# Kernel optimization log

Measured on AMD Instinct MI355X. Metric: run time of the kernel, lower is better.

The kernel has to match this reference:

```python
import jax, jax.numpy as jnp
import numpy as np
from jax import lax

SEQ_LEN = 256
INPUT_DIM = 1
HIDDEN = 1024
NUM_CLASSES = 10
BATCH = 512


def _kaiming_uniform(key, shape):
    # torch kaiming_uniform_ default: bound = sqrt(6 / fan_in), fan_in = shape[1]
    fan_in = shape[1]
    bound = float(np.sqrt(6.0 / fan_in))
    return jax.random.uniform(key, shape, jnp.float32, -bound, bound)


def setup_inputs() -> dict:
    key = jax.random.key(0)
    ks = jax.random.split(key, 16)
    inp = {"x": jax.random.normal(ks[0], (BATCH, SEQ_LEN), jnp.float32)}
    names_shapes = [
        ("Wgx", (HIDDEN, INPUT_DIM)), ("Wgh", (HIDDEN, HIDDEN)), ("bg", (HIDDEN, 1)),
        ("Wix", (HIDDEN, INPUT_DIM)), ("Wih", (HIDDEN, HIDDEN)), ("bi", (HIDDEN, 1)),
        ("Wfx", (HIDDEN, INPUT_DIM)), ("Wfh", (HIDDEN, HIDDEN)), ("bf", (HIDDEN, 1)),
        ("Wox", (HIDDEN, INPUT_DIM)), ("Woh", (HIDDEN, HIDDEN)), ("bo", (HIDDEN, 1)),
        ("Wph", (NUM_CLASSES, HIDDEN)), ("bp", (NUM_CLASSES, 1)),
    ]
    for k, (name, shape) in zip(ks[1:], names_shapes):
        inp[name] = _kaiming_uniform(k, shape)
    return inp


def reference(x, Wgx, Wgh, bg, Wix, Wih, bi, Wfx, Wfh, bf, Wox, Woh, bo, Wph, bp):
    B = x.shape[0]
    H = Wgh.shape[0]
    h0 = jnp.zeros((H, B), x.dtype)
    c0 = jnp.zeros((H, B), x.dtype)
    xs = x.T  # [S, B]; each step xt is [B] (input_dim == 1)

    def step(carry, xt):
        ht, ct = carry
        xt = xt[None, :]  # [1, B]
        g = jnp.tanh(Wgx @ xt + Wgh @ ht + bg)
        i = jax.nn.sigmoid(Wix @ xt + Wih @ ht + bi)
        f = jax.nn.sigmoid(Wfx @ xt + Wfh @ ht + bf)
        o = jax.nn.sigmoid(Wox @ xt + Woh @ ht + bo)
        ct = g * i + ct * f
        ht = jnp.tanh(ct) * o
        return (ht, ct), None

    (ht, ct), _ = lax.scan(step, (h0, c0), xs)
    pt = Wph @ ht + bp  # [num_classes, B], only last step's pt is returned
    return pt.T  # [B, num_classes]
```

## Files before the change

kernel.cpp:

```cpp
#include <hip/hip_runtime.h>


#define HID  1024
#define SEQL 256

typedef __bf16 bf16x8 __attribute__((ext_vector_type(8)));
typedef float  f32x16 __attribute__((ext_vector_type(16)));
typedef unsigned u32x4 __attribute__((ext_vector_type(4)));

#define AS1 __attribute__((address_space(1)))
#define AS3 __attribute__((address_space(3)))

__device__ __forceinline__ float fast_sigmoid(float v) {
    float e = __expf(-v);
    return 1.0f / (1.0f + e);
}
__device__ __forceinline__ float fast_tanh(float v) {
    float e = __expf(2.0f * v);
    return 1.0f - 2.0f / (e + 1.0f);
}
__device__ __forceinline__ unsigned pk2bf(float a, float b) {
    unsigned short ua = __builtin_bit_cast(unsigned short, (__bf16)a);
    unsigned short ub = __builtin_bit_cast(unsigned short, (__bf16)b);
    return (unsigned)ua | ((unsigned)ub << 16);
}
__device__ __forceinline__ float bfhi(unsigned u) { return __builtin_bit_cast(float, u & 0xFFFF0000u); }
__device__ __forceinline__ float bflo(unsigned u) { return __builtin_bit_cast(float, u << 16); }

__device__ __forceinline__ u32x4 load16_sc1(const void* p) {
    u32x4 r;
    asm volatile("global_load_dwordx4 %0, %1, off sc1\n\t"
                 "s_waitcnt vmcnt(0)"
                 : "=v"(r) : "v"(p) : "memory");
    return r;
}

__global__ __launch_bounds__(256) void lstm_init(unsigned short* htA, unsigned* flags, float* out) {
    int idx = blockIdx.x * 256 + threadIdx.x;
    uint4 z; z.x = 0; z.y = 0; z.z = 0; z.w = 0;
    ((uint4*)htA)[idx] = z;
    if (idx < 512) flags[idx] = 0;
    if (idx < 5120) out[idx] = 0.05f;
}

__global__ __attribute__((amdgpu_flat_work_group_size(256, 256), amdgpu_waves_per_eu(1, 1)))
void lstm_main(
    const float* __restrict__ x,
    const float* __restrict__ Wgx, const float* __restrict__ Wgh, const float* __restrict__ bg,
    const float* __restrict__ Wix, const float* __restrict__ Wih, const float* __restrict__ bi,
    const float* __restrict__ Wfx, const float* __restrict__ Wfh, const float* __restrict__ bf_,
    const float* __restrict__ Wox, const float* __restrict__ Woh, const float* __restrict__ bo,
    const float* __restrict__ Wph, const float* __restrict__ bp,
    float* __restrict__ out,
    unsigned short* __restrict__ htA, unsigned short* __restrict__ htB,
    unsigned* __restrict__ flags)
{
    extern __shared__ uint4 ldsB[];

    const int tid = threadIdx.x;
    const int w   = tid >> 6;
    const int l   = tid & 63;
    const int l31 = l & 31;
    const int h5  = l >> 5;
    const int gid = blockIdx.x;
    const int c   = gid & 7;
    const int r   = gid >> 3;

    const int gate = l31 >> 3;
    const int hrow = (r << 5) + (w << 3) + (l & 7);
    const float* Wsel = (gate == 0) ? Wgh : (gate == 1) ? Wih : (gate == 2) ? Wfh : Woh;
    const float* wrow = Wsel + hrow * HID + (h5 << 3);
    bf16x8 A[64];
#pragma unroll
    for (int kk = 0; kk < 64; ++kk) {
        const float4* p = (const float4*)(wrow + kk * 16);
        float4 u0 = p[0], u1 = p[1];
        bf16x8 a;
        a[0] = (__bf16)u0.x; a[1] = (__bf16)u0.y; a[2] = (__bf16)u0.z; a[3] = (__bf16)u0.w;
        a[4] = (__bf16)u1.x; a[5] = (__bf16)u1.y; a[6] = (__bf16)u1.z; a[7] = (__bf16)u1.w;
        A[kk] = a;
        __builtin_amdgcn_sched_barrier(0);
    }

    float wx16[16], bs16[16];
    {
        const float* WxA[4] = {Wgx, Wix, Wfx, Wox};
        const float* bA[4]  = {bg, bi, bf_, bo};
#pragma unroll
        for (int j = 0; j < 16; ++j) {
            int g = j >> 2;
            int h = (r << 5) + (w << 3) + (j & 3) + (h5 << 2);
            wx16[j] = WxA[g][h];
            bs16[j] = bA[g][h];
        }
    }

    float ct[8];
#pragma unroll
    for (int i = 0; i < 8; ++i) ct[i] = 0.f;

    const unsigned short* htR = htA;
    unsigned short*       htW = htB;
    unsigned* gflags = flags + (c << 6);
    const float* xrow0 = x + (unsigned)((c << 6) + l31) * SEQL;
    const float* xrow1 = x + (unsigned)((c << 6) + 32 + l31) * SEQL;

    float xv0 = xrow0[0], xv1 = xrow1[0];

    for (int t = 0; t < SEQL; ++t) {
        const unsigned short* gR = htR + (c << 16);

#pragma unroll
        for (int ch = 0; ch < 4; ++ch) {
#pragma unroll
            for (int j = 0; j < 8; ++j) {
                int q = (w << 3) + j;
                const void* g = (const void*)(gR + ch * 16384 + q * 512 + (l << 3));
                __builtin_amdgcn_global_load_lds((const AS1 void*)g,
                    (AS3 void*)&ldsB[(ch * 32 + q) * 64], 16, 0, 0x10 );
            }
        }
        __builtin_amdgcn_sched_barrier(0);
        int tn = (t + 1 < SEQL) ? t + 1 : t;
        float nx0 = xrow0[tn], nx1 = xrow1[tn];
        __builtin_amdgcn_sched_barrier(0);

        f32x16 acc0, acc1;
#pragma unroll
        for (int j = 0; j < 16; ++j) {
            acc0[j] = fmaf(wx16[j], xv0, bs16[j]);
            acc1[j] = fmaf(wx16[j], xv1, bs16[j]);
        }

#pragma unroll
        for (int ch = 0; ch < 4; ++ch) {
            if      (ch == 0) asm volatile("s_waitcnt vmcnt(24)" ::: "memory");
            else if (ch == 1) asm volatile("s_waitcnt vmcnt(16)" ::: "memory");
            else if (ch == 2) asm volatile("s_waitcnt vmcnt(8)"  ::: "memory");
            else              asm volatile("s_waitcnt vmcnt(2)"  ::: "memory");
            __builtin_amdgcn_s_barrier();
            asm volatile("" ::: "memory");
#pragma unroll
            for (int kk = 0; kk < 16; ++kk) {
                bf16x8 b0 = __builtin_bit_cast(bf16x8, ldsB[(ch * 32 + kk * 2 + 0) * 64 + l]);
                bf16x8 b1 = __builtin_bit_cast(bf16x8, ldsB[(ch * 32 + kk * 2 + 1) * 64 + l]);
                acc0 = __builtin_amdgcn_mfma_f32_32x32x16_bf16(A[ch * 16 + kk], b0, acc0, 0, 0, 0);
                acc1 = __builtin_amdgcn_mfma_f32_32x32x16_bf16(A[ch * 16 + kk], b1, acc1, 0, 0, 0);
            }
        }

        float htv[8];
#pragma unroll
        for (int nt = 0; nt < 2; ++nt) {
            f32x16 ac = nt ? acc1 : acc0;
#pragma unroll
            for (int d = 0; d < 4; ++d) {
                float g  = fast_tanh(ac[d]);
                float ii = fast_sigmoid(ac[4 + d]);
                float ff = fast_sigmoid(ac[8 + d]);
                float oo = fast_sigmoid(ac[12 + d]);
                float cc = fmaf(ct[nt * 4 + d], ff, g * ii);
                ct[nt * 4 + d] = cc;
                htv[nt * 4 + d] = fast_tanh(cc) * oo;
            }
        }

        {
            unsigned short* gW = htW + (c << 16);
            int kkw  = (r << 1) + (w >> 1);
            int slot = ((w & 1) << 5) + l31;
#pragma unroll
            for (int nt = 0; nt < 2; ++nt) {
                unsigned lo = pk2bf(htv[nt * 4 + 0], htv[nt * 4 + 1]);
                unsigned hi = pk2bf(htv[nt * 4 + 2], htv[nt * 4 + 3]);
                unsigned long long v = (unsigned long long)lo | ((unsigned long long)hi << 32);
                unsigned long long* dst =
                    (unsigned long long*)(gW + (((kkw * 2 + nt) * 64 + slot) * 8 + (h5 << 2)));
                __hip_atomic_store(dst, v, __ATOMIC_RELAXED, __HIP_MEMORY_SCOPE_AGENT);
            }
        }

        asm volatile("s_waitcnt vmcnt(0)" ::: "memory");
        __syncthreads();
        unsigned target = (unsigned)(t + 1);
        if (tid == 0)
            __hip_atomic_store(&gflags[r], target, __ATOMIC_RELAXED, __HIP_MEMORY_SCOPE_AGENT);
        if (w == 0) {
            const unsigned* fp = gflags + l31;
            while (true) {
                unsigned v = __hip_atomic_load(fp, __ATOMIC_RELAXED, __HIP_MEMORY_SCOPE_AGENT);
                if (__ballot(v >= target) == ~0ull) break;
                __builtin_amdgcn_s_sleep(1);
            }
        }
        __syncthreads();

        xv0 = nx0; xv1 = nx1;
        const unsigned short* tmp = htR; htR = htW; htW = (unsigned short*)tmp;
    }

    {
        const unsigned short* hfin = htR + (c << 16);
        for (int p = w; p < 20; p += 4) {
            int bloc = (r << 1) + (p / 10);
            int bb   = (c << 6) + bloc;
            int cls  = p % 10;
            const unsigned short* base = hfin + l * 1024 + ((bloc >> 5) & 1) * 512
                                              + (bloc & 31) * 8;
            u32x4 u0 = load16_sc1(base);
            u32x4 u1 = load16_sc1(base + 256);
            const float* wp = Wph + (unsigned)cls * HID + (unsigned)l * 16;
            float s = 0.f;
#pragma unroll
            for (int e = 0; e < 4; ++e) {
                s = fmaf(wp[2 * e],         bflo(u0[e]), s);
                s = fmaf(wp[2 * e + 1],     bfhi(u0[e]), s);
                s = fmaf(wp[8 + 2 * e],     bflo(u1[e]), s);
                s = fmaf(wp[8 + 2 * e + 1], bfhi(u1[e]), s);
            }
#pragma unroll
            for (int off = 32; off > 0; off >>= 1) s += __shfl_xor(s, off, 64);
            if (l == 0) out[bb * 10 + cls] = s + bp[cls];
        }
    }
}

extern "C" void kernel_launch(void* const* d_in, const int* in_sizes, int n_in,
                              void* d_out, int out_size, void* d_ws, size_t ws_size,
                              hipStream_t stream) {
    const float* x   = (const float*)d_in[0];
    const float* Wgx = (const float*)d_in[1];
    const float* Wgh = (const float*)d_in[2];
    const float* bg  = (const float*)d_in[3];
    const float* Wix = (const float*)d_in[4];
    const float* Wih = (const float*)d_in[5];
    const float* bi  = (const float*)d_in[6];
    const float* Wfx = (const float*)d_in[7];
    const float* Wfh = (const float*)d_in[8];
    const float* bf_ = (const float*)d_in[9];
    const float* Wox = (const float*)d_in[10];
    const float* Woh = (const float*)d_in[11];
    const float* bo  = (const float*)d_in[12];
    const float* Wph = (const float*)d_in[13];
    const float* bp  = (const float*)d_in[14];
    float* out = (float*)d_out;

    char* ws = (char*)d_ws;
    unsigned short* htA = (unsigned short*)ws;
    unsigned short* htB = (unsigned short*)(ws + (1 << 20));
    unsigned*     flags = (unsigned*)(ws + (2 << 20));

    lstm_init<<<dim3(256), dim3(256), 0, stream>>>(htA, flags, out);

    static int lds_set = 0;
    if (!lds_set) {
        hipFuncSetAttribute((const void*)lstm_main,
                            hipFuncAttributeMaxDynamicSharedMemorySize, 131072);
        lds_set = 1;
    }
    lstm_main<<<dim3(256), dim3(256), 131072, stream>>>(
        x, Wgx, Wgh, bg, Wix, Wih, bi, Wfx, Wfh, bf_,
        Wox, Woh, bo, Wph, bp, out, htA, htB, flags);
}
```

Before: 2.142 ms.

## Replace per-step block barriers with per-wave flags polled by every wave

The cross-workgroup handshake changes from one flag per workgroup, polled by wave 0 between two __syncthreads, to one flag per wave. Each wave polls all flags of its batch column with 64-bit loads at the start of the next step, and a final poll is added before the projection. Both __syncthreads per timestep are removed, and the hidden-state and flag stores become atomic exchanges. The aim is to cut intra-block barrier and serial-polling latency on the recurrent critical path, at the cost of more polling traffic and finer ordering that LDS and buffer reuse now depend on.

```diff
diff --git a/kernel.cpp b/kernel.cpp
--- a/kernel.cpp
+++ b/kernel.cpp
@@ -39,7 +39,7 @@
     int idx = blockIdx.x * 256 + threadIdx.x;
     uint4 z; z.x = 0; z.y = 0; z.z = 0; z.w = 0;
     ((uint4*)htA)[idx] = z;
-    if (idx < 512) flags[idx] = 0;
+    if (idx < 1024) flags[idx] = 0;
     if (idx < 5120) out[idx] = 0.05f;
 }
 
@@ -101,13 +101,26 @@
 
     const unsigned short* htR = htA;
     unsigned short*       htW = htB;
-    unsigned* gflags = flags + (c << 6);
+    unsigned* gflags = flags + (c << 7);
+    unsigned* myflag = gflags + (r << 2) + w;
+    const unsigned long long* pollp = (const unsigned long long*)gflags + l;
     const float* xrow0 = x + (unsigned)((c << 6) + l31) * SEQL;
     const float* xrow1 = x + (unsigned)((c << 6) + 32 + l31) * SEQL;
 
     float xv0 = xrow0[0], xv1 = xrow1[0];
 
     for (int t = 0; t < SEQL; ++t) {
+        unsigned target = (unsigned)t;
+        if (t > 0) {
+            while (true) {
+                unsigned long long v = __hip_atomic_load(pollp, __ATOMIC_RELAXED,
+                                                         __HIP_MEMORY_SCOPE_AGENT);
+                bool ok = ((unsigned)v >= target) && ((unsigned)(v >> 32) >= target);
+                if (__ballot(ok) == ~0ull) break;
+                __builtin_amdgcn_s_sleep(1);
+            }
+        }
+
         const unsigned short* gR = htR + (c << 16);
 
 #pragma unroll
@@ -134,9 +147,9 @@
 
 #pragma unroll
         for (int ch = 0; ch < 4; ++ch) {
-            if      (ch == 0) asm volatile("s_waitcnt vmcnt(24)" ::: "memory");
-            else if (ch == 1) asm volatile("s_waitcnt vmcnt(16)" ::: "memory");
-            else if (ch == 2) asm volatile("s_waitcnt vmcnt(8)"  ::: "memory");
+            if      (ch == 0) asm volatile("s_waitcnt vmcnt(26)" ::: "memory");
+            else if (ch == 1) asm volatile("s_waitcnt vmcnt(18)" ::: "memory");
+            else if (ch == 2) asm volatile("s_waitcnt vmcnt(10)" ::: "memory");
             else              asm volatile("s_waitcnt vmcnt(2)"  ::: "memory");
             __builtin_amdgcn_s_barrier();
             asm volatile("" ::: "memory");
@@ -176,27 +189,27 @@
                 unsigned long long v = (unsigned long long)lo | ((unsigned long long)hi << 32);
                 unsigned long long* dst =
                     (unsigned long long*)(gW + (((kkw * 2 + nt) * 64 + slot) * 8 + (h5 << 2)));
-                __hip_atomic_store(dst, v, __ATOMIC_RELAXED, __HIP_MEMORY_SCOPE_AGENT);
-            }
-        }
-
+                (void)__hip_atomic_exchange(dst, v, __ATOMIC_RELAXED, __HIP_MEMORY_SCOPE_AGENT);
+            }
+        }
         asm volatile("s_waitcnt vmcnt(0)" ::: "memory");
-        __syncthreads();
-        unsigned target = (unsigned)(t + 1);
-        if (tid == 0)
-            __hip_atomic_store(&gflags[r], target, __ATOMIC_RELAXED, __HIP_MEMORY_SCOPE_AGENT);
-        if (w == 0) {
-            const unsigned* fp = gflags + l31;
-            while (true) {
-                unsigned v = __hip_atomic_load(fp, __ATOMIC_RELAXED, __HIP_MEMORY_SCOPE_AGENT);
-                if (__ballot(v >= target) == ~0ull) break;
-                __builtin_amdgcn_s_sleep(1);
-            }
-        }
-        __syncthreads();
+        if (l == 0)
+            (void)__hip_atomic_exchange(myflag, (unsigned)(t + 1),
+                                        __ATOMIC_RELAXED, __HIP_MEMORY_SCOPE_AGENT);
 
         xv0 = nx0; xv1 = nx1;
         const unsigned short* tmp = htR; htR = htW; htW = (unsigned short*)tmp;
+    }
+
+    {
+        unsigned target = (unsigned)SEQL;
+        while (true) {
+            unsigned long long v = __hip_atomic_load(pollp, __ATOMIC_RELAXED,
+                                                     __HIP_MEMORY_SCOPE_AGENT);
+            bool ok = ((unsigned)v >= target) && ((unsigned)(v >> 32) >= target);
+            if (__ballot(ok) == ~0ull) break;
+            __builtin_amdgcn_s_sleep(1);
+        }
     }
 
     {
```

Measured after the change: 3.639 ms. 1.7x slower.

## Detect same-XCD block groups and use cheaper cache scope for hidden-state exchange

Applied to the files above, without the earlier changes.

At kernel start each block records its XCC ID and checks whether all 32 blocks sharing a batch column group run on the same XCD. If they do, the hidden-state loads switch from device-coherent (sc1) to XCD-local (sc0) scope and the stores become plain, so the exchange can be served from the shared L2 instead of going further out. The first timestep skips the recurrent GEMM because h0 is zero, which also removes the need to zero the ht buffer in the init kernel. This relies on the hardware block-to-XCD placement and adds a startup handshake, and correctness of the fast path depends on L2 coherence within an XCD.

```diff
diff --git a/kernel.cpp b/kernel.cpp
--- a/kernel.cpp
+++ b/kernel.cpp
@@ -27,19 +27,25 @@
 __device__ __forceinline__ float bfhi(unsigned u) { return __builtin_bit_cast(float, u & 0xFFFF0000u); }
 __device__ __forceinline__ float bflo(unsigned u) { return __builtin_bit_cast(float, u << 16); }
 
+__device__ __forceinline__ void store_sc1(unsigned* p, unsigned v) {
+    asm volatile("global_store_dword %0, %1, off sc1" :: "v"(p), "v"(v) : "memory");
+}
 __device__ __forceinline__ u32x4 load16_sc1(const void* p) {
     u32x4 r;
     asm volatile("global_load_dwordx4 %0, %1, off sc1\n\t"
-                 "s_waitcnt vmcnt(0)"
-                 : "=v"(r) : "v"(p) : "memory");
+                 "s_waitcnt vmcnt(0)" : "=v"(r) : "v"(p) : "memory");
     return r;
 }
-
-__global__ __launch_bounds__(256) void lstm_init(unsigned short* htA, unsigned* flags, float* out) {
+__device__ __forceinline__ u32x4 load16_sc0(const void* p) {
+    u32x4 r;
+    asm volatile("global_load_dwordx4 %0, %1, off sc0\n\t"
+                 "s_waitcnt vmcnt(0)" : "=v"(r) : "v"(p) : "memory");
+    return r;
+}
+
+__global__ __launch_bounds__(256) void lstm_init(unsigned* sync, float* out) {
     int idx = blockIdx.x * 256 + threadIdx.x;
-    uint4 z; z.x = 0; z.y = 0; z.z = 0; z.w = 0;
-    ((uint4*)htA)[idx] = z;
-    if (idx < 512) flags[idx] = 0;
+    if (idx < 768) store_sc1(sync + idx, 0u);
     if (idx < 5120) out[idx] = 0.05f;
 }
 
@@ -53,7 +59,7 @@
     const float* __restrict__ Wph, const float* __restrict__ bp,
     float* __restrict__ out,
     unsigned short* __restrict__ htA, unsigned short* __restrict__ htB,
-    unsigned* __restrict__ flags)
+    unsigned* __restrict__ sync)
 {
     extern __shared__ uint4 ldsB[];
 
@@ -95,35 +101,37 @@
         }
     }
 
+    unsigned xcd;
+    asm volatile("s_getreg_b32 %0, hwreg(HW_REG_XCC_ID)" : "=s"(xcd));
+    unsigned* xslot = sync + 512;
+    if (tid == 0) store_sc1(xslot + gid, xcd + 1u);
+    bool fast;
+    {
+        const unsigned* sp = xslot + c + (l31 << 3);
+        unsigned sv;
+        while (true) {
+            sv = __hip_atomic_load(sp, __ATOMIC_RELAXED, __HIP_MEMORY_SCOPE_AGENT);
+            if (__ballot(sv >= 1u && sv <= 8u) == ~0ull) break;
+            __builtin_amdgcn_s_sleep(1);
+        }
+        fast = (__ballot(sv == xcd + 1u) == ~0ull);
+    }
+
     float ct[8];
 #pragma unroll
     for (int i = 0; i < 8; ++i) ct[i] = 0.f;
 
     const unsigned short* htR = htA;
     unsigned short*       htW = htB;
-    unsigned* gflags = flags + (c << 6);
+    unsigned* gflags = sync + (c << 6);
     const float* xrow0 = x + (unsigned)((c << 6) + l31) * SEQL;
     const float* xrow1 = x + (unsigned)((c << 6) + 32 + l31) * SEQL;
 
     float xv0 = xrow0[0], xv1 = xrow1[0];
 
     for (int t = 0; t < SEQL; ++t) {
-        const unsigned short* gR = htR + (c << 16);
-
-#pragma unroll
-        for (int ch = 0; ch < 4; ++ch) {
-#pragma unroll
-            for (int j = 0; j < 8; ++j) {
-                int q = (w << 3) + j;
-                const void* g = (const void*)(gR + ch * 16384 + q * 512 + (l << 3));
-                __builtin_amdgcn_global_load_lds((const AS1 void*)g,
-                    (AS3 void*)&ldsB[(ch * 32 + q) * 64], 16, 0, 0x10 );
-            }
-        }
-        __builtin_amdgcn_sched_barrier(0);
         int tn = (t + 1 < SEQL) ? t + 1 : t;
         float nx0 = xrow0[tn], nx1 = xrow1[tn];
-        __builtin_amdgcn_sched_barrier(0);
 
         f32x16 acc0, acc1;
 #pragma unroll
@@ -132,20 +140,47 @@
             acc1[j] = fmaf(wx16[j], xv1, bs16[j]);
         }
 
-#pragma unroll
-        for (int ch = 0; ch < 4; ++ch) {
-            if      (ch == 0) asm volatile("s_waitcnt vmcnt(24)" ::: "memory");
-            else if (ch == 1) asm volatile("s_waitcnt vmcnt(16)" ::: "memory");
-            else if (ch == 2) asm volatile("s_waitcnt vmcnt(8)"  ::: "memory");
-            else              asm volatile("s_waitcnt vmcnt(2)"  ::: "memory");
-            __builtin_amdgcn_s_barrier();
-            asm volatile("" ::: "memory");
-#pragma unroll
-            for (int kk = 0; kk < 16; ++kk) {
-                bf16x8 b0 = __builtin_bit_cast(bf16x8, ldsB[(ch * 32 + kk * 2 + 0) * 64 + l]);
-                bf16x8 b1 = __builtin_bit_cast(bf16x8, ldsB[(ch * 32 + kk * 2 + 1) * 64 + l]);
-                acc0 = __builtin_amdgcn_mfma_f32_32x32x16_bf16(A[ch * 16 + kk], b0, acc0, 0, 0, 0);
-                acc1 = __builtin_amdgcn_mfma_f32_32x32x16_bf16(A[ch * 16 + kk], b1, acc1, 0, 0, 0);
+        if (t > 0) {
+            const unsigned short* gR = htR + (c << 16);
+
+            if (fast) {
+#pragma unroll
+                for (int ch = 0; ch < 4; ++ch)
+#pragma unroll
+                    for (int j = 0; j < 8; ++j) {
+                        int q = (w << 3) + j;
+                        const void* g = (const void*)(gR + ch * 16384 + q * 512 + (l << 3));
+                        __builtin_amdgcn_global_load_lds((const AS1 void*)g,
+                            (AS3 void*)&ldsB[(ch * 32 + q) * 64], 16, 0, 0x1 );
+                    }
+            } else {
+#pragma unroll
+                for (int ch = 0; ch < 4; ++ch)
+#pragma unroll
+                    for (int j = 0; j < 8; ++j) {
+                        int q = (w << 3) + j;
+                        const void* g = (const void*)(gR + ch * 16384 + q * 512 + (l << 3));
+                        __builtin_amdgcn_global_load_lds((const AS1 void*)g,
+                            (AS3 void*)&ldsB[(ch * 32 + q) * 64], 16, 0, 0x10 );
+                    }
+            }
+            __builtin_amdgcn_sched_barrier(0);
+
+#pragma unroll
+            for (int ch = 0; ch < 4; ++ch) {
+                if      (ch == 0) asm volatile("s_waitcnt vmcnt(24)" ::: "memory");
+                else if (ch == 1) asm volatile("s_waitcnt vmcnt(16)" ::: "memory");
+                else if (ch == 2) asm volatile("s_waitcnt vmcnt(8)"  ::: "memory");
+                else              asm volatile("s_waitcnt vmcnt(0)"  ::: "memory");
+                __builtin_amdgcn_s_barrier();
+                asm volatile("" ::: "memory");
+#pragma unroll
+                for (int kk = 0; kk < 16; ++kk) {
+                    bf16x8 b0 = __builtin_bit_cast(bf16x8, ldsB[(ch * 32 + kk * 2 + 0) * 64 + l]);
+                    bf16x8 b1 = __builtin_bit_cast(bf16x8, ldsB[(ch * 32 + kk * 2 + 1) * 64 + l]);
+                    acc0 = __builtin_amdgcn_mfma_f32_32x32x16_bf16(A[ch * 16 + kk], b0, acc0, 0, 0, 0);
+                    acc1 = __builtin_amdgcn_mfma_f32_32x32x16_bf16(A[ch * 16 + kk], b1, acc1, 0, 0, 0);
+                }
             }
         }
 
@@ -176,7 +211,8 @@
                 unsigned long long v = (unsigned long long)lo | ((unsigned long long)hi << 32);
                 unsigned long long* dst =
                     (unsigned long long*)(gW + (((kkw * 2 + nt) * 64 + slot) * 8 + (h5 << 2)));
-                __hip_atomic_store(dst, v, __ATOMIC_RELAXED, __HIP_MEMORY_SCOPE_AGENT);
+                if (fast) *dst = v;
+                else __hip_atomic_store(dst, v, __ATOMIC_RELAXED, __HIP_MEMORY_SCOPE_AGENT);
             }
         }
 
@@ -207,8 +243,9 @@
             int cls  = p % 10;
             const unsigned short* base = hfin + l * 1024 + ((bloc >> 5) & 1) * 512
                                               + (bloc & 31) * 8;
-            u32x4 u0 = load16_sc1(base);
-            u32x4 u1 = load16_sc1(base + 256);
+            u32x4 u0, u1;
+            if (fast) { u0 = load16_sc0(base); u1 = load16_sc0(base + 256); }
+            else      { u0 = load16_sc1(base); u1 = load16_sc1(base + 256); }
             const float* wp = Wph + (unsigned)cls * HID + (unsigned)l * 16;
             float s = 0.f;
 #pragma unroll
@@ -248,9 +285,9 @@
     char* ws = (char*)d_ws;
     unsigned short* htA = (unsigned short*)ws;
     unsigned short* htB = (unsigned short*)(ws + (1 << 20));
-    unsigned*     flags = (unsigned*)(ws + (2 << 20));
-
-    lstm_init<<<dim3(256), dim3(256), 0, stream>>>(htA, flags, out);
+    unsigned*      sync = (unsigned*)(ws + (2 << 20));
+
+    lstm_init<<<dim3(20), dim3(256), 0, stream>>>(sync, out);
 
     static int lds_set = 0;
     if (!lds_set) {
@@ -260,5 +297,5 @@
     }
     lstm_main<<<dim3(256), dim3(256), 131072, stream>>>(
         x, Wgx, Wgh, bg, Wix, Wih, bi, Wfx, Wfh, bf_,
-        Wox, Woh, bo, Wph, bp, out, htA, htB, flags);
-}
+        Wox, Woh, bo, Wph, bp, out, htA, htB, sync);
+}
```

New measurement: 1.764 ms. 1.21x faster.
